# Kernel optimization log

Hardware: AMD Instinct MI355X
Metric: run time of the kernel (lower is better)

The kernel has to match this reference:

```python
import jax, jax.numpy as jnp
import numpy as np

IN_F = 2048
OUT_F = 4096
LOW_DIM = 2048
LL_W = OUT_F * IN_F      # 8388608 = 2**23, power of two
LL_B = OUT_F             # 4096 = 2**12


def fwht(v):
    """Fast Walsh-Hadamard transform over a 1-D power-of-two vector (unnormalized),
    matching fast_walsh_hadamard_torched (chunk+cat butterfly)."""
    n = v.shape[0]
    k = int(round(np.log2(n)))
    v = v.reshape((2,) * k)
    for i in range(k):  # loop over log2(n) butterfly stages, not data dims
        a, b = jnp.split(v, 2, axis=i)
        v = jnp.concatenate([a + b, a - b], axis=i)
    return v.reshape(n)


def fastfood(z, dim, BB, GG, Pi):
    """pad -> sign-mul -> WHT -> permute -> Gaussian-mul -> WHT -> slice+scale."""
    LL = BB.shape[0]
    zp = jnp.zeros((LL,), z.dtype).at[: z.shape[0]].set(z)
    m = fwht(BB * zp)
    m = m[Pi] * GG
    m = fwht(m)
    divisor = jnp.sqrt(LL * jnp.sum(GG * GG))
    return m[:dim] / (divisor * np.sqrt(float(dim) / LL))


def setup_inputs() -> dict:
    key = jax.random.key(0)
    ks = jax.random.split(key, 9)
    x = jax.random.normal(ks[0], (4096, IN_F), dtype=jnp.float32)
    low_dim_params = jax.random.normal(ks[1], (LOW_DIM,), dtype=jnp.float32)
    W0 = jax.random.normal(ks[2], (OUT_F, IN_F), dtype=jnp.float32) * 0.02
    b0 = jax.random.normal(ks[3], (OUT_F,), dtype=jnp.float32) * 0.02
    # BB: random +/-1 signs (torch: uniform_(0,2).long()*2-1)
    BB_w = jnp.where(jax.random.uniform(ks[4], (LL_W,)) < 0.5, -1.0, 1.0).astype(jnp.float32)
    GG_w = jax.random.normal(ks[5], (LL_W,), dtype=jnp.float32)
    BB_b = jnp.where(jax.random.uniform(ks[6], (LL_B,)) < 0.5, -1.0, 1.0).astype(jnp.float32)
    GG_b = jax.random.normal(ks[7], (LL_B,), dtype=jnp.float32)
    kp1, kp2 = jax.random.split(ks[8])
    Pi_w = jax.random.permutation(kp1, LL_W).astype(jnp.int64)
    Pi_b = jax.random.permutation(kp2, LL_B).astype(jnp.int64)
    return {"x": x, "low_dim_params": low_dim_params, "W0": W0, "b0": b0,
            "BB_w": BB_w, "GG_w": GG_w, "BB_b": BB_b, "GG_b": GG_b,
            "Pi_w": Pi_w, "Pi_b": Pi_b}


def reference(x, low_dim_params, W0, b0, BB_w, GG_w, BB_b, GG_b, Pi_w, Pi_b):
    # FastfoodWrapper.set_params: param = initial_value + fastfood(low_dim_params)
    dW = fastfood(low_dim_params, OUT_F * IN_F, BB_w, GG_w, Pi_w).reshape(OUT_F, IN_F)
    db = fastfood(low_dim_params, OUT_F, BB_b, GG_b, Pi_b)
    W = W0 + dW
    b = b0 + db
    # base model forward: Linear
    return x @ W.T + b
```

## Files before the change

kernel.cpp:

```cpp
#include <hip/hip_runtime.h>
#include <hip/hip_bf16.h>
#include <math.h>

typedef __bf16  bf16x8 __attribute__((ext_vector_type(8)));
typedef float   f32x4  __attribute__((ext_vector_type(4)));

static __device__ __forceinline__ void load_lds16(const void* g, void* l) {
  __builtin_amdgcn_global_load_lds(
      (const __attribute__((address_space(1))) void*)(g),
      (__attribute__((address_space(3))) void*)(l), 16, 0, 0);
}

#define BAR() asm volatile("s_barrier" ::: "memory")
#define SB0() __builtin_amdgcn_sched_barrier(0)
#define LGKM(N) do { asm volatile("s_waitcnt lgkmcnt(" #N ")" ::: "memory"); SB0(); } while (0)
#define VMC(N) asm volatile("s_waitcnt vmcnt(" #N ")" ::: "memory")

static __device__ __forceinline__ float bf2f(unsigned short u) {
  unsigned int x = ((unsigned int)u) << 16;
  return __builtin_bit_cast(float, x);
}
static __device__ __forceinline__ unsigned short f2bf(float f) {
  __hip_bfloat16 h = __float2bfloat16(f);
  return *reinterpret_cast<unsigned short*>(&h);
}
static __device__ __forceinline__ unsigned pack2bf(float lo, float hi) {
  return (unsigned)f2bf(lo) | ((unsigned)f2bf(hi) << 16);
}

__global__ __launch_bounds__(256, 4) void k_mid1(
    const float* __restrict__ z, const float* __restrict__ BBw,
    const float* __restrict__ b0, const float* __restrict__ BBb,
    const float* __restrict__ GGb, const int* __restrict__ Pib,
    const int* __restrict__ Piw, const float* __restrict__ GGw,
    float* __restrict__ b_buf, float* __restrict__ Sw_part,
    __hip_bfloat16* __restrict__ m_buf) {
  __shared__ float S[4096];
  __shared__ float red[16];
  const int tid = threadIdx.x;
  const int bid = blockIdx.x;

  if (bid == 1024) {
    for (int i = tid; i < 4096; i += 256)
      S[i] = (i < 2048) ? BBb[i] * z[i] : 0.0f;
    float s = 0.0f;
    for (int i = tid; i < 4096; i += 256) { float g = GGb[i]; s += g * g; }
    for (int off = 32; off > 0; off >>= 1) s += __shfl_down(s, off);
    if ((tid & 63) == 0) red[tid >> 6] = s;
    __syncthreads();
    for (int len = 1; len < 4096; len <<= 1) {
      #pragma unroll
      for (int q = 0; q < 8; ++q) {
        int j = q * 256 + tid;
        int a = ((j & ~(len - 1)) << 1) | (j & (len - 1));
        float xx = S[a], y = S[a + len];
        S[a] = xx + y; S[a + len] = xx - y;
      }
      __syncthreads();
    }
    float v[16];
    #pragma unroll
    for (int q = 0; q < 16; ++q) v[q] = S[Pib[q * 256 + tid]] * GGb[q * 256 + tid];
    __syncthreads();
    #pragma unroll
    for (int q = 0; q < 16; ++q) S[q * 256 + tid] = v[q];
    __syncthreads();
    for (int len = 1; len < 4096; len <<= 1) {
      #pragma unroll
      for (int q = 0; q < 8; ++q) {
        int j = q * 256 + tid;
        int a = ((j & ~(len - 1)) << 1) | (j & (len - 1));
        float xx = S[a], y = S[a + len];
        S[a] = xx + y; S[a + len] = xx - y;
      }
      __syncthreads();
    }
    float Sb = red[0] + red[1] + red[2] + red[3];
    const float scale = 1.0f / sqrtf(Sb * 4096.0f);
    for (int i = tid; i < 4096; i += 256) b_buf[i] = b0[i] + S[i] * scale;
    return;
  }

  const int q6 = tid & 63, w = tid >> 6;

  {
    float v[8];
    float4 b0v = *reinterpret_cast<const float4*>(&BBw[tid * 8]);
    float4 b1v = *reinterpret_cast<const float4*>(&BBw[tid * 8 + 4]);
    float4 z0v = *reinterpret_cast<const float4*>(&z[tid * 8]);
    float4 z1v = *reinterpret_cast<const float4*>(&z[tid * 8 + 4]);
    v[0] = b0v.x * z0v.x; v[1] = b0v.y * z0v.y;
    v[2] = b0v.z * z0v.z; v[3] = b0v.w * z0v.w;
    v[4] = b1v.x * z1v.x; v[5] = b1v.y * z1v.y;
    v[6] = b1v.z * z1v.z; v[7] = b1v.w * z1v.w;
    #pragma unroll
    for (int st = 0; st < 3; ++st) {
      const int len = 1 << st;
      float t2[8];
      #pragma unroll
      for (int k = 0; k < 8; ++k) {
        int p = k ^ len;
        t2[k] = (k & len) ? v[p] - v[k] : v[k] + v[p];
      }
      #pragma unroll
      for (int k = 0; k < 8; ++k) v[k] = t2[k];
    }
    #pragma unroll
    for (int st = 0; st < 6; ++st) {
      const int xm = 1 << st;
      #pragma unroll
      for (int k = 0; k < 8; ++k) {
        float s2 = __shfl_xor(v[k], xm, 64);
        v[k] = (tid & xm) ? s2 - v[k] : v[k] + s2;
      }
    }
    #pragma unroll
    for (int k = 0; k < 8; ++k) S[2048 + k * 256 + tid] = v[k];
    __syncthreads();
    #pragma unroll
    for (int k = 0; k < 8; ++k) {
      float e0 = S[2048 + k * 256 + q6];
      float e1 = S[2048 + k * 256 + 64 + q6];
      float e2 = S[2048 + k * 256 + 128 + q6];
      float e3 = S[2048 + k * 256 + 192 + q6];
      float t1 = (w & 1) ? e0 - e1 : e0 + e1;
      float t2 = (w & 1) ? e2 - e3 : e2 + e3;
      v[k] = (w & 2) ? t1 - t2 : t1 + t2;
    }
    __syncthreads();
    f32x4 w0 = { v[0], v[1], v[2], v[3] };
    f32x4 w1 = { v[4], v[5], v[6], v[7] };
    *reinterpret_cast<f32x4*>(&S[tid * 8])     = w0;
    *reinterpret_cast<f32x4*>(&S[tid * 8 + 4]) = w1;
    __syncthreads();
  }

  float ssum = 0.0f;
  for (int rr = 0; rr < 4; ++rr) {
    const size_t p0 = ((size_t)bid * 4 + rr) * 2048;
    float v[8];
    #pragma unroll
    for (int h = 0; h < 2; ++h) {
      int4   pv = *reinterpret_cast<const int4*>(&Piw[p0 + tid * 8 + h * 4]);
      float4 gv = *reinterpret_cast<const float4*>(&GGw[p0 + tid * 8 + h * 4]);
      v[h * 4 + 0] = S[pv.x & 2047] * gv.x;
      v[h * 4 + 1] = S[pv.y & 2047] * gv.y;
      v[h * 4 + 2] = S[pv.z & 2047] * gv.z;
      v[h * 4 + 3] = S[pv.w & 2047] * gv.w;
      ssum += gv.x * gv.x + gv.y * gv.y + gv.z * gv.z + gv.w * gv.w;
    }
    #pragma unroll
    for (int st = 0; st < 3; ++st) {
      const int len = 1 << st;
      float t2[8];
      #pragma unroll
      for (int k = 0; k < 8; ++k) {
        int p = k ^ len;
        t2[k] = (k & len) ? v[p] - v[k] : v[k] + v[p];
      }
      #pragma unroll
      for (int k = 0; k < 8; ++k) v[k] = t2[k];
    }
    #pragma unroll
    for (int st = 0; st < 6; ++st) {
      const int xm = 1 << st;
      #pragma unroll
      for (int k = 0; k < 8; ++k) {
        float s2 = __shfl_xor(v[k], xm, 64);
        v[k] = (tid & xm) ? s2 - v[k] : v[k] + s2;
      }
    }
    #pragma unroll
    for (int k = 0; k < 8; ++k) S[2048 + k * 256 + tid] = v[k];
    __syncthreads();
    #pragma unroll
    for (int k = 0; k < 8; ++k) {
      float e0 = S[2048 + k * 256 + q6];
      float e1 = S[2048 + k * 256 + 64 + q6];
      float e2 = S[2048 + k * 256 + 128 + q6];
      float e3 = S[2048 + k * 256 + 192 + q6];
      float t1 = (w & 1) ? e0 - e1 : e0 + e1;
      float t2 = (w & 1) ? e2 - e3 : e2 + e3;
      v[k] = (w & 2) ? t1 - t2 : t1 + t2;
    }
    ushort4 o0 = make_ushort4(f2bf(v[0]), f2bf(v[1]), f2bf(v[2]), f2bf(v[3]));
    ushort4 o1 = make_ushort4(f2bf(v[4]), f2bf(v[5]), f2bf(v[6]), f2bf(v[7]));
    *reinterpret_cast<ushort4*>(&m_buf[p0 + tid * 8])     = o0;
    *reinterpret_cast<ushort4*>(&m_buf[p0 + tid * 8 + 4]) = o1;
    __syncthreads();
  }
  for (int off = 32; off > 0; off >>= 1) ssum += __shfl_down(ssum, off);
  if ((tid & 63) == 0) red[w] = ssum;
  __syncthreads();
  if (tid == 0) Sw_part[bid] = red[0] + red[1] + red[2] + red[3];
}

__global__ __launch_bounds__(256, 2) void k_mid2(__hip_bfloat16* __restrict__ m_buf,
                                                 const float* __restrict__ x,
                                                 __hip_bfloat16* __restrict__ xb,
                                                 const float* __restrict__ Sw_part,
                                                 float* __restrict__ Sw) {
  const int tid = threadIdx.x;
  const int gtid = blockIdx.x * 256 + tid;
  if (blockIdx.x == 0) {
    float s = 0.0f;
    for (int i = tid; i < 1024; i += 256) s += Sw_part[i];
    for (int off = 32; off > 0; off >>= 1) s += __shfl_down(s, off);
    __shared__ float r4[4];
    if ((tid & 63) == 0) r4[tid >> 6] = s;
    __syncthreads();
    if (tid == 0) *Sw = r4[0] + r4[1] + r4[2] + r4[3];
  }
  #pragma unroll
  for (int i = 0; i < 32; ++i) {
    int q = gtid + i * 65536;
    float4 xv = reinterpret_cast<const float4*>(x)[q];
    ushort4 pk = make_ushort4(f2bf(xv.x), f2bf(xv.y), f2bf(xv.z), f2bf(xv.w));
    reinterpret_cast<ushort4*>(xb)[q] = pk;
  }
  const int f2 = gtid & 1023, oh = gtid >> 10;
  unsigned* mp = reinterpret_cast<unsigned*>(m_buf);
  const size_t base = (size_t)oh * 65536 + (size_t)f2;
  float v0[64], v1[64];
  #pragma unroll
  for (int s = 0; s < 64; ++s) {
    unsigned u = mp[base + (size_t)s * 1024];
    v0[s] = bf2f((unsigned short)(u & 0xffff));
    v1[s] = bf2f((unsigned short)(u >> 16));
  }
  #pragma unroll
  for (int len = 1; len < 64; len <<= 1) {
    #pragma unroll
    for (int j = 0; j < 32; ++j) {
      int a = ((j & ~(len - 1)) << 1) | (j & (len - 1));
      float xx = v0[a], y = v0[a + len];
      v0[a] = xx + y; v0[a + len] = xx - y;
      float xx1 = v1[a], y1 = v1[a + len];
      v1[a] = xx1 + y1; v1[a + len] = xx1 - y1;
    }
  }
  #pragma unroll
  for (int s = 0; s < 64; ++s)
    mp[base + (size_t)s * 1024] = pack2bf(v0[s], v1[s]);
}

__global__ __launch_bounds__(256, 2) void k_mid3(const __hip_bfloat16* __restrict__ m_buf,
                                                 const float* __restrict__ W0,
                                                 const float* __restrict__ Sw,
                                                 __hip_bfloat16* __restrict__ Wb) {
  const int gtid = blockIdx.x * 256 + threadIdx.x;
  const int f2 = gtid & 1023, ol = gtid >> 10;
  const unsigned* mp = reinterpret_cast<const unsigned*>(m_buf);
  const size_t baseu = (size_t)ol * 1024 + (size_t)f2;
  float v0[64], v1[64];
  #pragma unroll
  for (int s = 0; s < 64; ++s) {
    unsigned u = mp[baseu + (size_t)s * 65536];
    v0[s] = bf2f((unsigned short)(u & 0xffff));
    v1[s] = bf2f((unsigned short)(u >> 16));
  }
  #pragma unroll
  for (int len = 1; len < 64; len <<= 1) {
    #pragma unroll
    for (int j = 0; j < 32; ++j) {
      int a = ((j & ~(len - 1)) << 1) | (j & (len - 1));
      float xx = v0[a], y = v0[a + len];
      v0[a] = xx + y; v0[a + len] = xx - y;
      float xx1 = v1[a], y1 = v1[a + len];
      v1[a] = xx1 + y1; v1[a + len] = xx1 - y1;
    }
  }
  const float scale = 1.0f / sqrtf((*Sw) * 8388608.0f);
  unsigned* wbu = reinterpret_cast<unsigned*>(Wb);
  #pragma unroll
  for (int s = 0; s < 64; ++s) {
    size_t eidx = ((size_t)ol * 2048 + (size_t)f2 * 2) + (size_t)s * 131072;
    float2 wv = *reinterpret_cast<const float2*>(&W0[eidx]);
    wbu[(eidx >> 1)] = pack2bf(wv.x + v0[s] * scale, wv.y + v1[s] * scale);
  }
}

__global__ __launch_bounds__(512, 2) void k_gemm(const __hip_bfloat16* __restrict__ A,
                                                 const __hip_bfloat16* __restrict__ B,
                                                 const float* __restrict__ bias,
                                                 float* __restrict__ C) {
  constexpr int K = 2048, N = 4096, NT = K / 64;
  __shared__ __hip_bfloat16 As[2][256 * 64];
  __shared__ __hip_bfloat16 Bs[2][256 * 64];
  const int tid = threadIdx.x;
  const int wave = tid >> 6, lane = tid & 63;
  const int bid = blockIdx.x;
  const int row0 = (bid & 15) * 256;
  const int col0 = (bid >> 4) * 256;
  const int wr = wave >> 2, wc = wave & 3;
  const int srow = tid >> 3;
  const int gslot = (tid & 7) ^ (srow & 7);
  const int ldst = tid * 8;
  const int lr = lane & 15, lk = lane >> 4;

  f32x4 acc[8][4] = {};
  bf16x8 a0[4][2], a1[4][2], b0[2][2], b1[2][2];

  #define STAGE_A(BUF, KT, CH0)                                                 \
    { _Pragma("unroll") for (int c = 0; c < 2; ++c)                             \
        load_lds16(A + (size_t)(row0 + (CH0 + c) * 64 + srow) * K + (KT) * 64 + gslot * 8, \
                   &As[BUF][(CH0 + c) * 4096 + ldst]); }
  #define STAGE_B(BUF, KT, CH0)                                                 \
    { _Pragma("unroll") for (int c = 0; c < 2; ++c)                             \
        load_lds16(B + (size_t)(col0 + (CH0 + c) * 64 + srow) * K + (KT) * 64 + gslot * 8, \
                   &Bs[BUF][(CH0 + c) * 4096 + ldst]); }

  #define READ_A(DST, BUF, HALF)                                                \
    { _Pragma("unroll") for (int i = 0; i < 4; ++i)                             \
        _Pragma("unroll") for (int ks = 0; ks < 2; ++ks) {                      \
          int row = wr * 128 + (HALF) * 64 + i * 16 + lr;                       \
          DST[i][ks] = *(const bf16x8*)&As[BUF][row * 64 + (((ks * 4 + lk) ^ (row & 7)) * 8)]; } }
  #define READ_B(DST, BUF, HALF)                                                \
    { _Pragma("unroll") for (int j = 0; j < 2; ++j)                             \
        _Pragma("unroll") for (int ks = 0; ks < 2; ++ks) {                      \
          int row = wc * 64 + (HALF) * 32 + j * 16 + lr;                        \
          DST[j][ks] = *(const bf16x8*)&Bs[BUF][row * 64 + (((ks * 4 + lk) ^ (row & 7)) * 8)]; } }

  #define MFMA16(AF, BF, IO, JO)                                                \
    { __builtin_amdgcn_s_setprio(1);                                            \
      _Pragma("unroll") for (int i = 0; i < 4; ++i)                             \
        _Pragma("unroll") for (int j = 0; j < 2; ++j)                           \
          _Pragma("unroll") for (int ks = 0; ks < 2; ++ks)                      \
            acc[(IO) + i][(JO) + j] =                                           \
              __builtin_amdgcn_mfma_f32_16x16x32_bf16(AF[i][ks], BF[j][ks],     \
                                                      acc[(IO) + i][(JO) + j], 0, 0, 0); \
      __builtin_amdgcn_s_setprio(0); }

  STAGE_A(0, 0, 0) STAGE_B(0, 0, 0) STAGE_A(0, 0, 2) STAGE_B(0, 0, 2)
  STAGE_A(1, 1, 0)
  VMC(2);
  BAR();

  for (int it = 0; it < 16; ++it) {
    const int u = 2 * it;
    const int v = u + 1;
    const int u2 = (u + 2 < NT) ? u + 2 : NT - 1;
    const int u3 = (u + 3 < NT) ? u + 3 : NT - 1;

    READ_A(a0, 0, 0) READ_B(b0, 0, 0)
    STAGE_A(1, v, 2)
    LGKM(8);
    BAR(); LGKM(0);
    MFMA16(a0, b0, 0, 0)
    VMC(4);
    BAR();
    READ_B(b1, 0, 1)
    STAGE_B(1, v, 0)
    BAR(); LGKM(0);
    MFMA16(a0, b1, 0, 2)
    BAR();
    READ_A(a1, 0, 1)
    STAGE_B(1, v, 2)
    BAR(); LGKM(0);
    MFMA16(a1, b1, 4, 2)
    BAR();
    STAGE_A(0, u2, 0)
    BAR();
    MFMA16(a1, b0, 4, 0)
    VMC(4);
    BAR();

    READ_A(a0, 1, 0) READ_B(b0, 1, 0)
    STAGE_B(0, u2, 0)
    LGKM(8);
    BAR(); LGKM(0);
    MFMA16(a0, b0, 0, 0)
    VMC(4);
    BAR();
    READ_B(b1, 1, 1)
    STAGE_A(0, u2, 2)
    BAR(); LGKM(0);
    MFMA16(a0, b1, 0, 2)
    BAR();
    READ_A(a1, 1, 1)
    STAGE_B(0, u2, 2)
    BAR(); LGKM(0);
    MFMA16(a1, b1, 4, 2)
    BAR();
    STAGE_A(1, u3, 0)
    BAR();
    MFMA16(a1, b0, 4, 0)
    VMC(6);
    BAR();
  }

  VMC(0);
  float bv[4];
  #pragma unroll
  for (int j = 0; j < 4; ++j) bv[j] = bias[col0 + wc * 64 + j * 16 + lr];
  float* eps = (float*)&As[0][0];
  #pragma unroll
  for (int r = 0; r < 4; ++r) {
    BAR();
    if (wr == (r >> 1)) {
      const int i0 = (r & 1) * 4;
      #pragma unroll
      for (int i = 0; i < 4; ++i)
        #pragma unroll
        for (int j = 0; j < 4; ++j)
          #pragma unroll
          for (int q = 0; q < 4; ++q) {
            int lrow = i * 16 + lk * 4 + q;
            int col = wc * 64 + j * 16 + lr;
            int sc = ((((col >> 2) ^ (lrow & 7)) << 2) | (col & 3));
            eps[lrow * 256 + sc] = acc[i0 + i][j][q] + bv[j];
          }
    }
    BAR();
    #pragma unroll
    for (int s = 0; s < 8; ++s) {
      int idx = s * 512 + tid;
      int lrow = idx >> 6;
      int g = idx & 63;
      f32x4 vv = *(const f32x4*)&eps[lrow * 256 + ((g ^ (lrow & 7)) << 2)];
      *(f32x4*)&C[(size_t)(row0 + r * 64 + lrow) * N + col0 + g * 4] = vv;
    }
  }
  #undef STAGE_A
  #undef STAGE_B
  #undef READ_A
  #undef READ_B
  #undef MFMA16
}

extern "C" void kernel_launch(void* const* d_in, const int* in_sizes, int n_in,
                              void* d_out, int out_size, void* d_ws, size_t ws_size,
                              hipStream_t stream) {
  (void)in_sizes; (void)n_in; (void)out_size; (void)ws_size;
  const float* x   = (const float*)d_in[0];
  const float* z   = (const float*)d_in[1];
  const float* W0  = (const float*)d_in[2];
  const float* b0  = (const float*)d_in[3];
  const float* BBw = (const float*)d_in[4];
  const float* GGw = (const float*)d_in[5];
  const float* BBb = (const float*)d_in[6];
  const float* GGb = (const float*)d_in[7];
  const int*   Piw = (const int*)d_in[8];
  const int*   Pib = (const int*)d_in[9];
  float* out = (float*)d_out;

  char* ws = (char*)d_ws;
  float*    b_buf   = (float*)(ws + 8192);
  float*    Sw      = (float*)(ws + 24576);
  float*    Sw_part = (float*)(ws + 28672);
  __hip_bfloat16* m_buf = (__hip_bfloat16*)(ws + 32768);
  __hip_bfloat16* Wb = (__hip_bfloat16*)(ws + 32768 + 16777216);
  __hip_bfloat16* xb = (__hip_bfloat16*)(ws + 32768 + 16777216 + 16777216);

  k_mid1<<<1025, 256, 0, stream>>>(z, BBw, b0, BBb, GGb, Pib, Piw, GGw,
                                   b_buf, Sw_part, m_buf);
  k_mid2<<<256, 256, 0, stream>>>(m_buf, x, xb, Sw_part, Sw);
  k_mid3<<<256, 256, 0, stream>>>(m_buf, W0, Sw, Wb);
  k_gemm<<<256, 512, 0, stream>>>(xb, Wb, b_buf, out);
}
```

Before: 127.8 us.

## Compute 2048-point WHT per wavefront in registers and move bias path to k_mid2

Result: slower. 133.2 us (+4.2%).

```diff
diff --git a/kernel.cpp b/kernel.cpp
--- a/kernel.cpp
+++ b/kernel.cpp
@@ -28,19 +28,107 @@
   return (unsigned)f2bf(lo) | ((unsigned)f2bf(hi) << 16);
 }
 
+static __device__ __forceinline__ void wht2048_lane(float v[32], int lane) {
+  #pragma unroll
+  for (int k = 0; k < 8; ++k) {
+    float a0 = v[k*4+0], a1 = v[k*4+1], a2 = v[k*4+2], a3 = v[k*4+3];
+    float b0 = a0 + a1, b1 = a0 - a1, b2 = a2 + a3, b3 = a2 - a3;
+    v[k*4+0] = b0 + b2; v[k*4+1] = b1 + b3;
+    v[k*4+2] = b0 - b2; v[k*4+3] = b1 - b3;
+  }
+  #pragma unroll
+  for (int j = 0; j < 6; ++j) {
+    const int m = 1 << j;
+    #pragma unroll
+    for (int r = 0; r < 32; ++r) {
+      float s2 = __shfl_xor(v[r], m, 64);
+      v[r] = (lane & m) ? s2 - v[r] : v[r] + s2;
+    }
+  }
+  #pragma unroll
+  for (int j = 0; j < 3; ++j) {
+    const int m = 1 << j;
+    #pragma unroll
+    for (int k = 0; k < 8; ++k) {
+      if (k & m) continue;
+      const int kp = k | m;
+      #pragma unroll
+      for (int i = 0; i < 4; ++i) {
+        float a = v[k*4+i], b = v[kp*4+i];
+        v[k*4+i] = a + b; v[kp*4+i] = a - b;
+      }
+    }
+  }
+}
+
 __global__ __launch_bounds__(256, 4) void k_mid1(
     const float* __restrict__ z, const float* __restrict__ BBw,
-    const float* __restrict__ b0, const float* __restrict__ BBb,
-    const float* __restrict__ GGb, const int* __restrict__ Pib,
     const int* __restrict__ Piw, const float* __restrict__ GGw,
-    float* __restrict__ b_buf, float* __restrict__ Sw_part,
-    __hip_bfloat16* __restrict__ m_buf) {
-  __shared__ float S[4096];
-  __shared__ float red[16];
+    float* __restrict__ Sw_part, __hip_bfloat16* __restrict__ m_buf) {
+  __shared__ float T[2048];
+  __shared__ float red[4];
+  const int tid = threadIdx.x, bid = blockIdx.x;
+  const int lane = tid & 63, w = tid >> 6;
+
+  float v[32];
+  #pragma unroll
+  for (int k = 0; k < 8; ++k) {
+    int e = k * 256 + lane * 4;
+    float4 bv = *reinterpret_cast<const float4*>(&BBw[e]);
+    float4 zv = *reinterpret_cast<const float4*>(&z[e]);
+    v[k*4+0] = bv.x * zv.x; v[k*4+1] = bv.y * zv.y;
+    v[k*4+2] = bv.z * zv.z; v[k*4+3] = bv.w * zv.w;
+  }
+  wht2048_lane(v, lane);
+  #pragma unroll
+  for (int k2 = 0; k2 < 2; ++k2) {
+    int k = w * 2 + k2;
+    f32x4 t4 = { v[k*4+0], v[k*4+1], v[k*4+2], v[k*4+3] };
+    *reinterpret_cast<f32x4*>(&T[k * 256 + lane * 4]) = t4;
+  }
+  __syncthreads();
+
+  const size_t p0 = ((size_t)bid * 4 + w) * 2048;
+  float ssum = 0.0f;
+  #pragma unroll
+  for (int k = 0; k < 8; ++k) {
+    int e = k * 256 + lane * 4;
+    int4   pv = *reinterpret_cast<const int4*>(&Piw[p0 + e]);
+    float4 gv = *reinterpret_cast<const float4*>(&GGw[p0 + e]);
+    v[k*4+0] = T[pv.x & 2047] * gv.x;
+    v[k*4+1] = T[pv.y & 2047] * gv.y;
+    v[k*4+2] = T[pv.z & 2047] * gv.z;
+    v[k*4+3] = T[pv.w & 2047] * gv.w;
+    ssum += gv.x*gv.x + gv.y*gv.y + gv.z*gv.z + gv.w*gv.w;
+  }
+  wht2048_lane(v, lane);
+  #pragma unroll
+  for (int k = 0; k < 8; ++k) {
+    ushort4 o = make_ushort4(f2bf(v[k*4+0]), f2bf(v[k*4+1]),
+                             f2bf(v[k*4+2]), f2bf(v[k*4+3]));
+    *reinterpret_cast<ushort4*>(&m_buf[p0 + k * 256 + lane * 4]) = o;
+  }
+  for (int off = 32; off > 0; off >>= 1) ssum += __shfl_down(ssum, off);
+  if (lane == 0) red[w] = ssum;
+  __syncthreads();
+  if (tid == 0) Sw_part[bid] = red[0] + red[1] + red[2] + red[3];
+}
+
+__global__ __launch_bounds__(256, 2) void k_mid2(__hip_bfloat16* __restrict__ m_buf,
+                                                 const float* __restrict__ x,
+                                                 __hip_bfloat16* __restrict__ xb,
+                                                 const float* __restrict__ Sw_part,
+                                                 float* __restrict__ Sw,
+                                                 const float* __restrict__ z,
+                                                 const float* __restrict__ b0,
+                                                 const float* __restrict__ BBb,
+                                                 const float* __restrict__ GGb,
+                                                 const int* __restrict__ Pib,
+                                                 float* __restrict__ b_buf) {
   const int tid = threadIdx.x;
-  const int bid = blockIdx.x;
-
-  if (bid == 1024) {
+  if (blockIdx.x == 256) {
+    __shared__ float S[4096];
+    __shared__ float red[16];
     for (int i = tid; i < 4096; i += 256)
       S[i] = (i < 2048) ? BBb[i] * z[i] : 0.0f;
     float s = 0.0f;
@@ -81,126 +169,6 @@
     return;
   }
 
-  const int q6 = tid & 63, w = tid >> 6;
-
-  {
-    float v[8];
-    float4 b0v = *reinterpret_cast<const float4*>(&BBw[tid * 8]);
-    float4 b1v = *reinterpret_cast<const float4*>(&BBw[tid * 8 + 4]);
-    float4 z0v = *reinterpret_cast<const float4*>(&z[tid * 8]);
-    float4 z1v = *reinterpret_cast<const float4*>(&z[tid * 8 + 4]);
-    v[0] = b0v.x * z0v.x; v[1] = b0v.y * z0v.y;
-    v[2] = b0v.z * z0v.z; v[3] = b0v.w * z0v.w;
-    v[4] = b1v.x * z1v.x; v[5] = b1v.y * z1v.y;
-    v[6] = b1v.z * z1v.z; v[7] = b1v.w * z1v.w;
-    #pragma unroll
-    for (int st = 0; st < 3; ++st) {
-      const int len = 1 << st;
-      float t2[8];
-      #pragma unroll
-      for (int k = 0; k < 8; ++k) {
-        int p = k ^ len;
-        t2[k] = (k & len) ? v[p] - v[k] : v[k] + v[p];
-      }
-      #pragma unroll
-      for (int k = 0; k < 8; ++k) v[k] = t2[k];
-    }
-    #pragma unroll
-    for (int st = 0; st < 6; ++st) {
-      const int xm = 1 << st;
-      #pragma unroll
-      for (int k = 0; k < 8; ++k) {
-        float s2 = __shfl_xor(v[k], xm, 64);
-        v[k] = (tid & xm) ? s2 - v[k] : v[k] + s2;
-      }
-    }
-    #pragma unroll
-    for (int k = 0; k < 8; ++k) S[2048 + k * 256 + tid] = v[k];
-    __syncthreads();
-    #pragma unroll
-    for (int k = 0; k < 8; ++k) {
-      float e0 = S[2048 + k * 256 + q6];
-      float e1 = S[2048 + k * 256 + 64 + q6];
-      float e2 = S[2048 + k * 256 + 128 + q6];
-      float e3 = S[2048 + k * 256 + 192 + q6];
-      float t1 = (w & 1) ? e0 - e1 : e0 + e1;
-      float t2 = (w & 1) ? e2 - e3 : e2 + e3;
-      v[k] = (w & 2) ? t1 - t2 : t1 + t2;
-    }
-    __syncthreads();
-    f32x4 w0 = { v[0], v[1], v[2], v[3] };
-    f32x4 w1 = { v[4], v[5], v[6], v[7] };
-    *reinterpret_cast<f32x4*>(&S[tid * 8])     = w0;
-    *reinterpret_cast<f32x4*>(&S[tid * 8 + 4]) = w1;
-    __syncthreads();
-  }
-
-  float ssum = 0.0f;
-  for (int rr = 0; rr < 4; ++rr) {
-    const size_t p0 = ((size_t)bid * 4 + rr) * 2048;
-    float v[8];
-    #pragma unroll
-    for (int h = 0; h < 2; ++h) {
-      int4   pv = *reinterpret_cast<const int4*>(&Piw[p0 + tid * 8 + h * 4]);
-      float4 gv = *reinterpret_cast<const float4*>(&GGw[p0 + tid * 8 + h * 4]);
-      v[h * 4 + 0] = S[pv.x & 2047] * gv.x;
-      v[h * 4 + 1] = S[pv.y & 2047] * gv.y;
-      v[h * 4 + 2] = S[pv.z & 2047] * gv.z;
-      v[h * 4 + 3] = S[pv.w & 2047] * gv.w;
-      ssum += gv.x * gv.x + gv.y * gv.y + gv.z * gv.z + gv.w * gv.w;
-    }
-    #pragma unroll
-    for (int st = 0; st < 3; ++st) {
-      const int len = 1 << st;
-      float t2[8];
-      #pragma unroll
-      for (int k = 0; k < 8; ++k) {
-        int p = k ^ len;
-        t2[k] = (k & len) ? v[p] - v[k] : v[k] + v[p];
-      }
-      #pragma unroll
-      for (int k = 0; k < 8; ++k) v[k] = t2[k];
-    }
-    #pragma unroll
-    for (int st = 0; st < 6; ++st) {
-      const int xm = 1 << st;
-      #pragma unroll
-      for (int k = 0; k < 8; ++k) {
-        float s2 = __shfl_xor(v[k], xm, 64);
-        v[k] = (tid & xm) ? s2 - v[k] : v[k] + s2;
-      }
-    }
-    #pragma unroll
-    for (int k = 0; k < 8; ++k) S[2048 + k * 256 + tid] = v[k];
-    __syncthreads();
-    #pragma unroll
-    for (int k = 0; k < 8; ++k) {
-      float e0 = S[2048 + k * 256 + q6];
-      float e1 = S[2048 + k * 256 + 64 + q6];
-      float e2 = S[2048 + k * 256 + 128 + q6];
-      float e3 = S[2048 + k * 256 + 192 + q6];
-      float t1 = (w & 1) ? e0 - e1 : e0 + e1;
-      float t2 = (w & 1) ? e2 - e3 : e2 + e3;
-      v[k] = (w & 2) ? t1 - t2 : t1 + t2;
-    }
-    ushort4 o0 = make_ushort4(f2bf(v[0]), f2bf(v[1]), f2bf(v[2]), f2bf(v[3]));
-    ushort4 o1 = make_ushort4(f2bf(v[4]), f2bf(v[5]), f2bf(v[6]), f2bf(v[7]));
-    *reinterpret_cast<ushort4*>(&m_buf[p0 + tid * 8])     = o0;
-    *reinterpret_cast<ushort4*>(&m_buf[p0 + tid * 8 + 4]) = o1;
-    __syncthreads();
-  }
-  for (int off = 32; off > 0; off >>= 1) ssum += __shfl_down(ssum, off);
-  if ((tid & 63) == 0) red[w] = ssum;
-  __syncthreads();
-  if (tid == 0) Sw_part[bid] = red[0] + red[1] + red[2] + red[3];
-}
-
-__global__ __launch_bounds__(256, 2) void k_mid2(__hip_bfloat16* __restrict__ m_buf,
-                                                 const float* __restrict__ x,
-                                                 __hip_bfloat16* __restrict__ xb,
-                                                 const float* __restrict__ Sw_part,
-                                                 float* __restrict__ Sw) {
-  const int tid = threadIdx.x;
   const int gtid = blockIdx.x * 256 + tid;
   if (blockIdx.x == 0) {
     float s = 0.0f;
@@ -452,9 +420,9 @@
   __hip_bfloat16* Wb = (__hip_bfloat16*)(ws + 32768 + 16777216);
   __hip_bfloat16* xb = (__hip_bfloat16*)(ws + 32768 + 16777216 + 16777216);
 
-  k_mid1<<<1025, 256, 0, stream>>>(z, BBw, b0, BBb, GGb, Pib, Piw, GGw,
-                                   b_buf, Sw_part, m_buf);
-  k_mid2<<<256, 256, 0, stream>>>(m_buf, x, xb, Sw_part, Sw);
+  k_mid1<<<1024, 256, 0, stream>>>(z, BBw, Piw, GGw, Sw_part, m_buf);
+  k_mid2<<<257, 256, 0, stream>>>(m_buf, x, xb, Sw_part, Sw,
+                                  z, b0, BBb, GGb, Pib, b_buf);
   k_mid3<<<256, 256, 0, stream>>>(m_buf, W0, Sw, Wb);
   k_gemm<<<256, 512, 0, stream>>>(xb, Wb, b_buf, out);
 }
```
